# Kernel tuning notes

Hardware: AMD Instinct MI355X
Metric: run time of the kernel (lower is better)

The kernel has to match this reference:

```python
import jax, jax.numpy as jnp
import numpy as np

B, H, W = 16, 128, 128
D = 64          # embedding_dim
K = 1024        # num_embeddings
CC = 0.25       # commitment_cost
KLD = 10.0      # kld_scale


def setup_inputs() -> dict:
    key = jax.random.key(0)
    k1, k2, k3, k4, k5, k6 = jax.random.split(key, 6)
    # xavier-uniform-ish codebook init
    lim = float(np.sqrt(6.0 / (K + D)))
    return {
        "x": jax.random.normal(k1, (B, 1, H, W), dtype=jnp.float32),
        "w_in": jax.random.normal(k2, (D,), dtype=jnp.float32),   # Conv2d(1,D,1) weight
        "b_in": jax.random.normal(k3, (D,), dtype=jnp.float32) * 0.1,
        "emb": jax.random.uniform(k4, (K, D), dtype=jnp.float32, minval=-lim, maxval=lim),
        "w_out": jax.random.normal(k5, (D,), dtype=jnp.float32),  # Conv2d(D,1,1) weight
        "b_out": jax.random.normal(k6, (1,), dtype=jnp.float32) * 0.1,
    }


def reference(x, w_in, b_in, emb, w_out, b_out):
    sg = jax.lax.stop_gradient
    # in_proj: 1x1 conv with 1 input channel == per-pixel scale+bias, NCHW -> NHWC-D
    h = x[:, 0, :, :, None] * w_in + b_in               # [B,H,W,D]
    flat = h.reshape(-1, D)                             # [N,D]
    # squared L2 distances to codebook: ||f||^2 - 2 f.e + ||e||^2
    dist = (jnp.sum(flat * flat, axis=1, keepdims=True)
            - 2.0 * flat @ emb.T
            + jnp.sum(emb * emb, axis=1))               # [N,K]
    idx = jnp.argmin(dist, axis=1).reshape(B, H, W)     # nearest code
    q = emb[idx]                                        # [B,H,W,D] gather
    emb_loss = KLD * (CC * jnp.mean((sg(q) - h) ** 2)
                      + jnp.mean((q - sg(h)) ** 2))
    q_st = h + sg(q - h)                                # straight-through
    # out_proj: 1x1 conv D->1
    out = (jnp.einsum("bhwd,d->bhw", q_st, w_out) + b_out[0])[:, None]  # [B,1,H,W]
    return out, emb_loss
```

## Files before the change

### kernel.cpp

```cpp
#include <hip/hip_runtime.h>


#define VQ_K 1024
#define VQ_D 64
#define NPIX 262144

__global__ void k_coeff(const float* __restrict__ emb, const float* __restrict__ w_in,
                        const float* __restrict__ b_in, const float* __restrict__ w_out,
                        double* __restrict__ ws) {
    int k = blockIdx.x * blockDim.x + threadIdx.x;
    if (k < VQ_K) {
        const float* e = emb + k * VQ_D;
        double p = 0.0, r = 0.0, c = 0.0, t = 0.0;
        for (int d = 0; d < VQ_D; ++d) {
            double ed = (double)e[d];
            p += ed * (double)w_in[d];
            r += ed * (double)b_in[d];
            c += ed * ed;
            t += ed * (double)w_out[d];
        }
        ws[k]        = c - 2.0 * r;
        ws[1024 + k] = -2.0 * p;
        ws[2048 + k] = t;
    }
    if (blockIdx.x == 0 && threadIdx.x == 0) {
        double W2 = 0.0, WB = 0.0, B2 = 0.0;
        for (int d = 0; d < VQ_D; ++d) {
            double w = (double)w_in[d], b = (double)b_in[d];
            W2 += w * w; WB += w * b; B2 += b * b;
        }
        ws[6144] = W2; ws[6145] = WB; ws[6146] = B2;
        ws[6147] = 0.0;
    }
}

__global__ void k_interval(double* __restrict__ ws) {
    const double* A = ws;
    const double* M = ws + 1024;
    int k = blockIdx.x;
    double ak = A[k], mk = M[k];
    double lo = -1e300, hi = 1e300;
    int dom = 0;
    for (int j = threadIdx.x; j < VQ_K; j += 256) {
        if (j == k) continue;
        double aj = A[j], mj = M[j];
        if (mj == mk) {
            if (aj < ak || (aj == ak && j < k)) dom = 1;
        } else {
            double xx = (aj - ak) / (mk - mj);
            if (mj > mk) lo = fmax(lo, xx);
            else         hi = fmin(hi, xx);
        }
    }
    __shared__ double slo[256], shi[256];
    __shared__ int sd[256];
    slo[threadIdx.x] = lo; shi[threadIdx.x] = hi; sd[threadIdx.x] = dom;
    __syncthreads();
    for (int s = 128; s > 0; s >>= 1) {
        if (threadIdx.x < s) {
            slo[threadIdx.x] = fmax(slo[threadIdx.x], slo[threadIdx.x + s]);
            shi[threadIdx.x] = fmin(shi[threadIdx.x], shi[threadIdx.x + s]);
            sd[threadIdx.x] |= sd[threadIdx.x + s];
        }
        __syncthreads();
    }
    if (threadIdx.x == 0) {
        double L = slo[0], R = shi[0];
        if (sd[0]) { L = 1e300; R = -1e300; }
        ws[3072 + k] = L;
        ws[4096 + k] = R;
    }
}

__global__ void k_rank(double* __restrict__ ws) {
    const double* L = ws + 3072;
    const double* R = ws + 4096;
    int k = blockIdx.x;
    double lk = L[k];
    int validk = (lk < R[k]) ? 1 : 0;
    int less = 0, nvalid = 0;
    for (int j = threadIdx.x; j < VQ_K; j += 256) {
        double lj = L[j];
        int vj = (lj < R[j]) ? 1 : 0;
        nvalid += vj;
        if (vj && (lj < lk || (lj == lk && j < k))) less++;
    }
    __shared__ int sl[256], sv[256];
    sl[threadIdx.x] = less; sv[threadIdx.x] = nvalid;
    __syncthreads();
    for (int s = 128; s > 0; s >>= 1) {
        if (threadIdx.x < s) {
            sl[threadIdx.x] += sl[threadIdx.x + s];
            sv[threadIdx.x] += sv[threadIdx.x + s];
        }
        __syncthreads();
    }
    if (threadIdx.x == 0) {
        int* C = (int*)(ws + 6152);
        if (validk) {
            int r = sl[0];
            C[r] = k;
            ws[5120 + r] = lk;
        }
        if (k == 0) C[1024] = sv[0];
    }
}

__global__ __launch_bounds__(256) void k_main(const float* __restrict__ x,
                                              const float* __restrict__ b_out,
                                              double* __restrict__ ws,
                                              float* __restrict__ out) {
    __shared__ double sT[VQ_K], sBP[VQ_K], sA[VQ_K], sM[VQ_K];
    __shared__ int sC[VQ_K];
    __shared__ double red[4];
    for (int i = threadIdx.x; i < VQ_K; i += 256) {
        sA[i]  = ws[i];
        sM[i]  = ws[1024 + i];
        sT[i]  = ws[2048 + i];
        sBP[i] = ws[5120 + i];
        sC[i]  = ((const int*)(ws + 6152))[i];
    }
    int S = ((const int*)(ws + 6152))[1024];
    double W2 = ws[6144], WB = ws[6145], B2 = ws[6146];
    double bo = (double)b_out[0];
    __syncthreads();

    int pix = blockIdx.x * 256 + threadIdx.x;
    double xv = (double)x[pix];

    int lo = 0, hi = S - 1;
    while (lo < hi) {
        int mid = (lo + hi + 1) >> 1;
        if (sBP[mid] <= xv) lo = mid; else hi = mid - 1;
    }
    int k = sC[lo];

    out[pix] = (float)(sT[k] + bo);

    double s = sA[k] + xv * sM[k] + xv * xv * W2 + 2.0 * xv * WB + B2;

    for (int off = 32; off > 0; off >>= 1) s += __shfl_down(s, off, 64);
    int lane = threadIdx.x & 63, wid = threadIdx.x >> 6;
    if (lane == 0) red[wid] = s;
    __syncthreads();
    if (threadIdx.x == 0) {
        double bs = red[0] + red[1] + red[2] + red[3];
        atomicAdd(&ws[6147], bs);
    }
}

__global__ void k_final(const double* __restrict__ ws, float* __restrict__ out) {
    out[NPIX] = (float)(12.5 * ws[6147] / 16777216.0);
}

extern "C" void kernel_launch(void* const* d_in, const int* in_sizes, int n_in,
                              void* d_out, int out_size, void* d_ws, size_t ws_size,
                              hipStream_t stream) {
    const float* x     = (const float*)d_in[0];
    const float* w_in  = (const float*)d_in[1];
    const float* b_in  = (const float*)d_in[2];
    const float* emb   = (const float*)d_in[3];
    const float* w_out = (const float*)d_in[4];
    const float* b_out = (const float*)d_in[5];
    float* out = (float*)d_out;
    double* ws = (double*)d_ws;

    hipLaunchKernelGGL(k_coeff,    dim3(4),    dim3(256), 0, stream, emb, w_in, b_in, w_out, ws);
    hipLaunchKernelGGL(k_interval, dim3(VQ_K), dim3(256), 0, stream, ws);
    hipLaunchKernelGGL(k_rank,     dim3(VQ_K), dim3(256), 0, stream, ws);
    hipLaunchKernelGGL(k_main,     dim3(NPIX / 256), dim3(256), 0, stream, x, b_out, ws, out);
    hipLaunchKernelGGL(k_final,    dim3(1),    dim3(1),   0, stream, ws, out);
}
```

Baseline: 95.38 us.

## Replace breakpoint ranking with linear scan over compacted envelope codes

Removes the ranking kernel and the final kernel. The interval kernel now compacts the codes that are ever the argmin into a dense list using an atomic counter. The per-pixel kernel processes four pixels per thread with float4 loads and takes a linear min over the S surviving lines instead of a binary search over sorted breakpoints. The loss is finalised by the last block, using a completion counter. This trades log-S search for O(S) FMA work per pixel. Because slots are assigned in atomic order, tie-breaking between equal values is no longer by lowest code index.

```diff
diff --git a/kernel.cpp b/kernel.cpp
--- a/kernel.cpp
+++ b/kernel.cpp
@@ -1,13 +1,14 @@
 #include <hip/hip_runtime.h>
+#include <hip/hip_bf16.h>
 
 
 #define VQ_K 1024
 #define VQ_D 64
 #define NPIX 262144
 
-__global__ void k_coeff(const float* __restrict__ emb, const float* __restrict__ w_in,
-                        const float* __restrict__ b_in, const float* __restrict__ w_out,
-                        double* __restrict__ ws) {
+__global__ void k_prep(const float* __restrict__ emb, const float* __restrict__ w_in,
+                       const float* __restrict__ b_in, const float* __restrict__ w_out,
+                       double* __restrict__ ws) {
     int k = blockIdx.x * blockDim.x + threadIdx.x;
     if (k < VQ_K) {
         const float* e = emb + k * VQ_D;
@@ -31,10 +32,13 @@
         }
         ws[6144] = W2; ws[6145] = WB; ws[6146] = B2;
         ws[6147] = 0.0;
+        int* cnt = (int*)(ws + 6148);
+        cnt[0] = 0;
+        cnt[1] = 0;
     }
 }
 
-__global__ void k_interval(double* __restrict__ ws) {
+__global__ void k_env(double* __restrict__ ws) {
     const double* A = ws;
     const double* M = ws + 1024;
     int k = blockIdx.x;
@@ -64,80 +68,58 @@
         }
         __syncthreads();
     }
-    if (threadIdx.x == 0) {
-        double L = slo[0], R = shi[0];
-        if (sd[0]) { L = 1e300; R = -1e300; }
-        ws[3072 + k] = L;
-        ws[4096 + k] = R;
+    if (threadIdx.x == 0 && !sd[0] && slo[0] < shi[0]) {
+        int* cnt = (int*)(ws + 6148);
+        int s = atomicAdd(&cnt[0], 1);
+        ws[3072 + s] = ak;
+        ws[4096 + s] = mk;
+        ws[5120 + s] = ws[2048 + k];
     }
 }
 
-__global__ void k_rank(double* __restrict__ ws) {
-    const double* L = ws + 3072;
-    const double* R = ws + 4096;
-    int k = blockIdx.x;
-    double lk = L[k];
-    int validk = (lk < R[k]) ? 1 : 0;
-    int less = 0, nvalid = 0;
-    for (int j = threadIdx.x; j < VQ_K; j += 256) {
-        double lj = L[j];
-        int vj = (lj < R[j]) ? 1 : 0;
-        nvalid += vj;
-        if (vj && (lj < lk || (lj == lk && j < k))) less++;
+__global__ __launch_bounds__(256) void k_pix(const float* __restrict__ x,
+                                             const float* __restrict__ b_out,
+                                             double* __restrict__ ws,
+                                             float* __restrict__ out) {
+    __shared__ double sA[VQ_K], sM[VQ_K], sT[VQ_K];
+    __shared__ double red[4];
+    int* cnt = (int*)(ws + 6148);
+    int S = cnt[0];
+    for (int i = threadIdx.x; i < S; i += 256) {
+        sA[i] = ws[3072 + i];
+        sM[i] = ws[4096 + i];
+        sT[i] = ws[5120 + i];
     }
-    __shared__ int sl[256], sv[256];
-    sl[threadIdx.x] = less; sv[threadIdx.x] = nvalid;
-    __syncthreads();
-    for (int s = 128; s > 0; s >>= 1) {
-        if (threadIdx.x < s) {
-            sl[threadIdx.x] += sl[threadIdx.x + s];
-            sv[threadIdx.x] += sv[threadIdx.x + s];
-        }
-        __syncthreads();
-    }
-    if (threadIdx.x == 0) {
-        int* C = (int*)(ws + 6152);
-        if (validk) {
-            int r = sl[0];
-            C[r] = k;
-            ws[5120 + r] = lk;
-        }
-        if (k == 0) C[1024] = sv[0];
-    }
-}
-
-__global__ __launch_bounds__(256) void k_main(const float* __restrict__ x,
-                                              const float* __restrict__ b_out,
-                                              double* __restrict__ ws,
-                                              float* __restrict__ out) {
-    __shared__ double sT[VQ_K], sBP[VQ_K], sA[VQ_K], sM[VQ_K];
-    __shared__ int sC[VQ_K];
-    __shared__ double red[4];
-    for (int i = threadIdx.x; i < VQ_K; i += 256) {
-        sA[i]  = ws[i];
-        sM[i]  = ws[1024 + i];
-        sT[i]  = ws[2048 + i];
-        sBP[i] = ws[5120 + i];
-        sC[i]  = ((const int*)(ws + 6152))[i];
-    }
-    int S = ((const int*)(ws + 6152))[1024];
     double W2 = ws[6144], WB = ws[6145], B2 = ws[6146];
     double bo = (double)b_out[0];
     __syncthreads();
 
-    int pix = blockIdx.x * 256 + threadIdx.x;
-    double xv = (double)x[pix];
+    int gid = blockIdx.x * 256 + threadIdx.x;
+    float4 xv4 = ((const float4*)x)[gid];
+    double xv[4] = {(double)xv4.x, (double)xv4.y, (double)xv4.z, (double)xv4.w};
+    double best[4] = {1e300, 1e300, 1e300, 1e300};
+    double bt[4]   = {0.0, 0.0, 0.0, 0.0};
 
-    int lo = 0, hi = S - 1;
-    while (lo < hi) {
-        int mid = (lo + hi + 1) >> 1;
-        if (sBP[mid] <= xv) lo = mid; else hi = mid - 1;
+    for (int s = 0; s < S; ++s) {
+        double a = sA[s], m = sM[s], t = sT[s];
+        #pragma unroll
+        for (int p = 0; p < 4; ++p) {
+            double v = fma(xv[p], m, a);
+            if (v < best[p]) { best[p] = v; bt[p] = t; }
+        }
     }
-    int k = sC[lo];
 
-    out[pix] = (float)(sT[k] + bo);
+    float4 o;
+    o.x = (float)(bt[0] + bo);
+    o.y = (float)(bt[1] + bo);
+    o.z = (float)(bt[2] + bo);
+    o.w = (float)(bt[3] + bo);
+    ((float4*)out)[gid] = o;
 
-    double s = sA[k] + xv * sM[k] + xv * xv * W2 + 2.0 * xv * WB + B2;
+    double s = 0.0;
+    #pragma unroll
+    for (int p = 0; p < 4; ++p)
+        s += best[p] + xv[p] * xv[p] * W2 + 2.0 * xv[p] * WB + B2;
 
     for (int off = 32; off > 0; off >>= 1) s += __shfl_down(s, off, 64);
     int lane = threadIdx.x & 63, wid = threadIdx.x >> 6;
@@ -146,11 +128,13 @@
     if (threadIdx.x == 0) {
         double bs = red[0] + red[1] + red[2] + red[3];
         atomicAdd(&ws[6147], bs);
+        __threadfence();
+        int old = atomicAdd(&cnt[1], 1);
+        if (old == (int)gridDim.x - 1) {
+            double total = atomicAdd(&ws[6147], 0.0);
+            out[NPIX] = (float)(12.5 * total / 16777216.0);
+        }
     }
-}
-
-__global__ void k_final(const double* __restrict__ ws, float* __restrict__ out) {
-    out[NPIX] = (float)(12.5 * ws[6147] / 16777216.0);
 }
 
 extern "C" void kernel_launch(void* const* d_in, const int* in_sizes, int n_in,
@@ -165,9 +149,7 @@
     float* out = (float*)d_out;
     double* ws = (double*)d_ws;
 
-    hipLaunchKernelGGL(k_coeff,    dim3(4),    dim3(256), 0, stream, emb, w_in, b_in, w_out, ws);
-    hipLaunchKernelGGL(k_interval, dim3(VQ_K), dim3(256), 0, stream, ws);
-    hipLaunchKernelGGL(k_rank,     dim3(VQ_K), dim3(256), 0, stream, ws);
-    hipLaunchKernelGGL(k_main,     dim3(NPIX / 256), dim3(256), 0, stream, x, b_out, ws, out);
-    hipLaunchKernelGGL(k_final,    dim3(1),    dim3(1),   0, stream, ws, out);
+    hipLaunchKernelGGL(k_prep, dim3(4),         dim3(256), 0, stream, emb, w_in, b_in, w_out, ws);
+    hipLaunchKernelGGL(k_env,  dim3(VQ_K),      dim3(256), 0, stream, ws);
+    hipLaunchKernelGGL(k_pix,  dim3(NPIX/1024), dim3(256), 0, stream, x, b_out, ws, out);
 }
```

New measurement: 82.99 us. 13.0% less time.
